# Kernel optimization log

Measured on AMD Instinct MI355X. Metric: run time of the kernel, lower is better.

Reference implementation:

```python
import jax, jax.numpy as jnp
import numpy as np

B, C, H, Wd = 4096, 32, 14, 14
ENC_DIM = 512
ATT_DIM = 128


def setup_inputs() -> dict:
    key = jax.random.key(0)
    ks = jax.random.split(key, 10)
    s = 0.05
    return {
        "img_features": jax.random.normal(ks[0], (B, C, H, Wd), jnp.float32),
        "prev_hidden": jax.random.normal(ks[1], (B, ENC_DIM), jnp.float32),
        "W_w": jax.random.normal(ks[2], (ATT_DIM, C), jnp.float32) * s,
        "W_b": jnp.zeros((ATT_DIM,), jnp.float32),
        "U_w": jax.random.normal(ks[3], (ATT_DIM, ENC_DIM), jnp.float32) * s,
        "U_b": jnp.zeros((ATT_DIM,), jnp.float32),
        "v_w": jax.random.normal(ks[4], (1, ATT_DIM), jnp.float32) * s,
        "v_b": jnp.zeros((1,), jnp.float32),
        "fb_w": jax.random.normal(ks[5], (C, ENC_DIM), jnp.float32) * s,
        "fb_b": jnp.zeros((C,), jnp.float32),
    }


def reference(img_features, prev_hidden, W_w, W_b, U_w, U_b, v_w, v_b, fb_w, fb_b):
    b = img_features.shape[0]
    c = img_features.shape[1]
    # [B, C, H, W] -> [B, P, C] where P = H*W (spatial positions)
    img_parts = img_features.reshape(b, c, -1).transpose(0, 2, 1)
    W_s = jnp.einsum('bpc,ac->bpa', img_parts, W_w) + W_b          # [B, P, 128]
    U_h = prev_hidden @ U_w.T + U_b                                 # [B, 128]
    att = jnp.tanh(W_s + U_h[:, None, :])                           # [B, P, 128]
    score = jnp.einsum('bpa,a->bp', att, v_w[0]) + v_b[0]           # [B, P]
    att_weights = jax.nn.softmax(score, axis=1)                     # softmax over spatial
    context = jnp.einsum('bpc,bp->bc', img_parts, att_weights)      # [B, 32]
    beta = jax.nn.sigmoid(prev_hidden @ fb_w.T + fb_b)              # [B, 32]
    context = context * beta
    return (context, att_weights)
```

## Files before the change

kernel.cpp:

```cpp
#include <hip/hip_runtime.h>
#include <hip/hip_bf16.h>


typedef __attribute__((ext_vector_type(8))) short short8;
typedef __attribute__((ext_vector_type(8))) __bf16 bf16x8;
typedef __attribute__((ext_vector_type(4))) float floatx4;
typedef __attribute__((ext_vector_type(4))) unsigned int uint4v;

static __device__ __forceinline__ float bf2f(unsigned short u) {
    union { unsigned int i; float f; } v; v.i = ((unsigned int)u) << 16; return v.f;
}
static __device__ __forceinline__ unsigned short f2bf(float f) {
    union { float f; unsigned int i; } v; v.f = f;
    unsigned int r = v.i + 0x7FFFu + ((v.i >> 16) & 1u);
    return (unsigned short)(r >> 16);
}
static __device__ __forceinline__ float tanh_rcp(float x) {
    float e = __expf(2.0f * x);
    float r = __builtin_amdgcn_rcpf(1.0f + e);
    return __builtin_fmaf(-2.0f, r, 1.0f);
}
static __device__ __forceinline__ float sigmoid_rcp(float x) {
    return __builtin_amdgcn_rcpf(1.0f + __expf(-x));
}
static __device__ __forceinline__ void split_trunc8(const float* src, bf16x8* hi, bf16x8* lo) {
    uint4v u0 = *(const uint4v*)src;
    uint4v u1 = *(const uint4v*)(src + 4);
    unsigned int fb[8], lb[8];
#pragma unroll
    for (int j = 0; j < 4; j++) { fb[j] = u0[j]; fb[4 + j] = u1[j]; }
#pragma unroll
    for (int k = 0; k < 8; k++) {
        float x = __uint_as_float(fb[k]);
        float h = __uint_as_float(fb[k] & 0xFFFF0000u);
        lb[k] = __float_as_uint(x - h);
    }
    uint4v hp, lp;
#pragma unroll
    for (int j = 0; j < 4; j++) {
        hp[j] = __builtin_amdgcn_perm(fb[2 * j + 1], fb[2 * j], 0x07060302u);
        lp[j] = __builtin_amdgcn_perm(lb[2 * j + 1], lb[2 * j], 0x07060302u);
    }
    *hi = __builtin_bit_cast(bf16x8, hp);
    *lo = __builtin_bit_cast(bf16x8, lp);
}

__global__ __launch_bounds__(256) void k0_split(
    const float* __restrict__ U_w, const float* __restrict__ fb_w,
    const float* __restrict__ W_w,
    unsigned short* __restrict__ Bhi, unsigned short* __restrict__ Blo,
    unsigned short* __restrict__ Whi, unsigned short* __restrict__ Wlo)
{
    int i = blockIdx.x * 256 + threadIdx.x;
    float x;
    if (i < 65536) x = U_w[i];
    else if (i < 81920) x = fb_w[i - 65536];
    else x = W_w[i - 81920];
    unsigned short h = f2bf(x);
    unsigned short l = f2bf(x - bf2f(h));
    if (i < 81920) { Bhi[i] = h; Blo[i] = l; }
    else { Whi[i - 81920] = h; Wlo[i - 81920] = l; }
}

__global__ __launch_bounds__(256) void k1_gemm(
    const float* __restrict__ hidden,
    const unsigned short* __restrict__ Bhi,
    const unsigned short* __restrict__ Blo,
    const float* __restrict__ U_b, const float* __restrict__ W_b,
    const float* __restrict__ fb_b,
    float* __restrict__ uh_out, float* __restrict__ beta_out,
    float* __restrict__ partial, int nsplit, int direct)
{
    __shared__ float s_part[4 * 2560];
    const int tid = threadIdx.x;
    const int wave = tid >> 6, lane = tid & 63, quad = lane >> 4, l16 = lane & 15;
    const int mtile = blockIdx.x / nsplit;
    const int kblock = 512 / nsplit;
    const int ks0 = (blockIdx.x % nsplit) * kblock + wave * (kblock >> 2);
    const int ksteps = kblock >> 7;
    const int arow = mtile * 16 + l16;

    floatx4 acc[10];
#pragma unroll
    for (int i = 0; i < 10; i++) acc[i] = (floatx4)(0.0f);

    for (int ksi = 0; ksi < ksteps; ksi++) {
        const int e0 = ks0 + ksi * 32 + quad * 8;
        bf16x8 ah, al;
        split_trunc8(hidden + (size_t)arow * 512 + e0, &ah, &al);
#pragma unroll
        for (int n = 0; n < 10; n++) {
            const size_t bo = (size_t)(n * 16 + l16) * 512 + e0;
            bf16x8 bh = *(const bf16x8*)(Bhi + bo);
            bf16x8 bl = *(const bf16x8*)(Blo + bo);
            acc[n] = __builtin_amdgcn_mfma_f32_16x16x32_bf16(ah, bl, acc[n], 0, 0, 0);
            acc[n] = __builtin_amdgcn_mfma_f32_16x16x32_bf16(al, bh, acc[n], 0, 0, 0);
            acc[n] = __builtin_amdgcn_mfma_f32_16x16x32_bf16(ah, bh, acc[n], 0, 0, 0);
        }
    }
#pragma unroll
    for (int n = 0; n < 10; n++)
#pragma unroll
        for (int r = 0; r < 4; r++)
            s_part[wave * 2560 + (quad * 4 + r) * 160 + n * 16 + l16] = acc[n][r];
    __syncthreads();

#pragma unroll
    for (int j = 0; j < 10; j++) {
        const int i = tid + j * 256;
        float v = s_part[i] + s_part[2560 + i] + s_part[5120 + i] + s_part[7680 + i];
        if (direct) {
            const int m = mtile * 16 + i / 160, col = i % 160;
            if (col < 128) uh_out[(size_t)m * 128 + col] = v + U_b[col] + W_b[col];
            else beta_out[(size_t)m * 32 + (col - 128)] = sigmoid_rcp(v + fb_b[col - 128]);
        } else {
            partial[(size_t)blockIdx.x * 2560 + i] = v;
        }
    }
}

__global__ __launch_bounds__(256) void k1b_reduce(
    const float* __restrict__ partial,
    const float* __restrict__ U_b, const float* __restrict__ W_b,
    const float* __restrict__ fb_b,
    float* __restrict__ uh_out, float* __restrict__ beta_out, int nsplit)
{
    const int idx = blockIdx.x * 256 + threadIdx.x;
    const int mt = idx / 2560, r = idx % 2560;
    float v = 0.0f;
    for (int s = 0; s < nsplit; s++)
        v += partial[(size_t)(mt * nsplit + s) * 2560 + r];
    const int m = mt * 16 + r / 160, col = r % 160;
    if (col < 128) uh_out[(size_t)m * 128 + col] = v + U_b[col] + W_b[col];
    else beta_out[(size_t)m * 32 + (col - 128)] = sigmoid_rcp(v + fb_b[col - 128]);
}

#define FSTR 36

__global__ __launch_bounds__(256, 4) void k2_attn(
    const float* __restrict__ img,
    const unsigned short* __restrict__ Whi,
    const unsigned short* __restrict__ Wlo,
    const float* __restrict__ v_w,
    const float* __restrict__ uh,
    const float* __restrict__ beta,
    float* __restrict__ out)
{
    __shared__ __align__(16) float s_img[208 * FSTR];
    __shared__ float s_uhv[256];
    __shared__ float s_score[200];
    __shared__ float s_red[8];
    __shared__ float s_ctx[4][32];

    const int tid = threadIdx.x;
    const int b = blockIdx.x;
    const int wave = tid >> 6, lane = tid & 63, quad = lane >> 4, l16 = lane & 15;

    if (tid < 196) {
        const size_t base = (size_t)b * 6272 + tid;
#pragma unroll
        for (int g = 0; g < 8; g++) {
            floatx4 t;
#pragma unroll
            for (int j = 0; j < 4; j++) t[j] = img[base + (size_t)(4 * g + j) * 196];
            *(floatx4*)&s_img[tid * FSTR + 4 * g] = t;
        }
    } else {
        for (int i = tid - 196; i < 12 * FSTR; i += 60) s_img[196 * FSTR + i] = 0.0f;
    }
    if (tid < 128) s_uhv[tid] = uh[(size_t)b * 128 + tid];
    else s_uhv[tid] = v_w[tid - 128];

    bf16x8 bh[8], bl[8];
#pragma unroll
    for (int nt = 0; nt < 8; nt++) {
        const int a = nt * 16 + l16;
        bh[nt] = *(const bf16x8*)(Whi + a * 32 + quad * 8);
        bl[nt] = *(const bf16x8*)(Wlo + a * 32 + quad * 8);
    }
    __syncthreads();

    float ua[8], va[8];
#pragma unroll
    for (int nt = 0; nt < 8; nt++) {
        ua[nt] = s_uhv[nt * 16 + l16];
        va[nt] = s_uhv[128 + nt * 16 + l16];
    }

    for (int mt = wave; mt < 13; mt += 4) {
        const int p_lane = mt * 16 + l16;
        bf16x8 ah, al;
        split_trunc8(&s_img[p_lane * FSTR + quad * 8], &ah, &al);
        float sc[4] = {0.f, 0.f, 0.f, 0.f};
#pragma unroll
        for (int nt = 0; nt < 8; nt++) {
            floatx4 d = (floatx4)(0.0f);
            d = __builtin_amdgcn_mfma_f32_16x16x32_bf16(ah, bl[nt], d, 0, 0, 0);
            d = __builtin_amdgcn_mfma_f32_16x16x32_bf16(al, bh[nt], d, 0, 0, 0);
            d = __builtin_amdgcn_mfma_f32_16x16x32_bf16(ah, bh[nt], d, 0, 0, 0);
#pragma unroll
            for (int r = 0; r < 4; r++)
                sc[r] = __builtin_fmaf(va[nt], tanh_rcp(d[r] + ua[nt]), sc[r]);
        }
#pragma unroll
        for (int r = 0; r < 4; r++) {
            sc[r] += __shfl_xor(sc[r], 1);
            sc[r] += __shfl_xor(sc[r], 2);
            sc[r] += __shfl_xor(sc[r], 4);
            sc[r] += __shfl_xor(sc[r], 8);
        }
        if (l16 == 0) {
#pragma unroll
            for (int r = 0; r < 4; r++) {
                const int p = mt * 16 + quad * 4 + r;
                if (p < 196) s_score[p] = sc[r];
            }
        }
    }
    __syncthreads();

    float x = (tid < 196) ? s_score[tid] : -1e30f;
    float m = x;
#pragma unroll
    for (int off = 32; off > 0; off >>= 1) m = fmaxf(m, __shfl_xor(m, off));
    if (lane == 0) s_red[wave] = m;
    __syncthreads();
    m = fmaxf(fmaxf(s_red[0], s_red[1]), fmaxf(s_red[2], s_red[3]));
    float e = (tid < 196) ? __expf(x - m) : 0.0f;
    float ssum = e;
#pragma unroll
    for (int off = 32; off > 0; off >>= 1) ssum += __shfl_xor(ssum, off);
    if (lane == 0) s_red[4 + wave] = ssum;
    __syncthreads();
    const float tot = s_red[4] + s_red[5] + s_red[6] + s_red[7];
    const float wgt = e * __builtin_amdgcn_rcpf(tot);
    if (tid < 196) {
        s_score[tid] = wgt;
        out[131072 + (size_t)b * 196 + tid] = wgt;
    }
    __syncthreads();

    {
        const int c = lane & 31;
        const int po = wave * 2 + (lane >> 5);
        float acc = 0.0f;
        for (int j = 0; j < 25; j++) {
            const int p = po + j * 8;
            if (p < 196) acc = __builtin_fmaf(s_img[p * FSTR + c], s_score[p], acc);
        }
        acc += __shfl_xor(acc, 32);
        if ((lane >> 5) == 0) s_ctx[wave][c] = acc;
    }
    __syncthreads();
    if (tid < 32) {
        const float v = s_ctx[0][tid] + s_ctx[1][tid] + s_ctx[2][tid] + s_ctx[3][tid];
        out[(size_t)b * 32 + tid] = v * beta[(size_t)b * 32 + tid];
    }
}

extern "C" void kernel_launch(void* const* d_in, const int* in_sizes, int n_in,
                              void* d_out, int out_size, void* d_ws, size_t ws_size,
                              hipStream_t stream) {
    const float* img    = (const float*)d_in[0];
    const float* hidden = (const float*)d_in[1];
    const float* W_w    = (const float*)d_in[2];
    const float* W_b    = (const float*)d_in[3];
    const float* U_w    = (const float*)d_in[4];
    const float* U_b    = (const float*)d_in[5];
    const float* v_w    = (const float*)d_in[6];
    const float* fb_w   = (const float*)d_in[8];
    const float* fb_b   = (const float*)d_in[9];
    float* out = (float*)d_out;

    float* uh_ws   = (float*)d_ws;
    float* beta_ws = uh_ws + 4096 * 128;
    unsigned short* Bhi = (unsigned short*)(beta_ws + 4096 * 32);
    unsigned short* Blo = Bhi + 81920;
    unsigned short* Whi = Blo + 81920;
    unsigned short* Wlo = Whi + 4096;
    float* partial = (float*)(Wlo + 4096);
    const size_t fixed_bytes = ((char*)partial) - ((char*)d_ws);

    int nsplit = 1, direct = 1;
    if (ws_size >= fixed_bytes + (size_t)256 * 4 * 2560 * 4) { nsplit = 4; direct = 0; }
    else if (ws_size >= fixed_bytes + (size_t)256 * 2 * 2560 * 4) { nsplit = 2; direct = 0; }
    else if (ws_size >= fixed_bytes + (size_t)256 * 1 * 2560 * 4) { nsplit = 1; direct = 0; }

    k0_split<<<dim3(336), dim3(256), 0, stream>>>(U_w, fb_w, W_w, Bhi, Blo, Whi, Wlo);
    k1_gemm<<<dim3(256 * nsplit), dim3(256), 0, stream>>>(
        hidden, Bhi, Blo, U_b, W_b, fb_b, uh_ws, beta_ws, partial, nsplit, direct);
    if (!direct)
        k1b_reduce<<<dim3(2560), dim3(256), 0, stream>>>(
            partial, U_b, W_b, fb_b, uh_ws, beta_ws, nsplit);
    k2_attn<<<dim3(4096), dim3(256), 0, stream>>>(img, Whi, Wlo, v_w, uh_ws, beta_ws, out);
}
```

Before: 211.7 us.

## Fold tanh scaling into weights, restructure MFMA loop over m-tiles

```diff
diff --git a/kernel.cpp b/kernel.cpp
--- a/kernel.cpp
+++ b/kernel.cpp
@@ -7,6 +7,14 @@
 typedef __attribute__((ext_vector_type(4))) float floatx4;
 typedef __attribute__((ext_vector_type(4))) unsigned int uint4v;
 
+#define K2E 2.8853900817779268f
+
+#if __has_builtin(__builtin_amdgcn_exp2f)
+#define EXP2F(x) __builtin_amdgcn_exp2f(x)
+#else
+#define EXP2F(x) __expf(0.6931471805599453f * (x))
+#endif
+
 static __device__ __forceinline__ float bf2f(unsigned short u) {
     union { unsigned int i; float f; } v; v.i = ((unsigned int)u) << 16; return v.f;
 }
@@ -15,11 +23,6 @@
     unsigned int r = v.i + 0x7FFFu + ((v.i >> 16) & 1u);
     return (unsigned short)(r >> 16);
 }
-static __device__ __forceinline__ float tanh_rcp(float x) {
-    float e = __expf(2.0f * x);
-    float r = __builtin_amdgcn_rcpf(1.0f + e);
-    return __builtin_fmaf(-2.0f, r, 1.0f);
-}
 static __device__ __forceinline__ float sigmoid_rcp(float x) {
     return __builtin_amdgcn_rcpf(1.0f + __expf(-x));
 }
@@ -43,6 +46,11 @@
     }
     *hi = __builtin_bit_cast(bf16x8, hp);
     *lo = __builtin_bit_cast(bf16x8, lp);
+}
+static __device__ __forceinline__ void pinv(bf16x8& v) {
+    uint4v u = __builtin_bit_cast(uint4v, v);
+    asm volatile("" : "+v"(u));
+    v = __builtin_bit_cast(bf16x8, u);
 }
 
 __global__ __launch_bounds__(256) void k0_split(
@@ -55,7 +63,7 @@
     float x;
     if (i < 65536) x = U_w[i];
     else if (i < 81920) x = fb_w[i - 65536];
-    else x = W_w[i - 81920];
+    else x = W_w[i - 81920] * K2E;
     unsigned short h = f2bf(x);
     unsigned short l = f2bf(x - bf2f(h));
     if (i < 81920) { Bhi[i] = h; Blo[i] = l; }
@@ -64,8 +72,7 @@
 
 __global__ __launch_bounds__(256) void k1_gemm(
     const float* __restrict__ hidden,
-    const unsigned short* __restrict__ Bhi,
-    const unsigned short* __restrict__ Blo,
+    const unsigned short* __restrict__ Bhi, const unsigned short* __restrict__ Blo,
     const float* __restrict__ U_b, const float* __restrict__ W_b,
     const float* __restrict__ fb_b,
     float* __restrict__ uh_out, float* __restrict__ beta_out,
@@ -111,7 +118,7 @@
         float v = s_part[i] + s_part[2560 + i] + s_part[5120 + i] + s_part[7680 + i];
         if (direct) {
             const int m = mtile * 16 + i / 160, col = i % 160;
-            if (col < 128) uh_out[(size_t)m * 128 + col] = v + U_b[col] + W_b[col];
+            if (col < 128) uh_out[(size_t)m * 128 + col] = K2E * (v + U_b[col] + W_b[col]);
             else beta_out[(size_t)m * 32 + (col - 128)] = sigmoid_rcp(v + fb_b[col - 128]);
         } else {
             partial[(size_t)blockIdx.x * 2560 + i] = v;
@@ -131,7 +138,7 @@
     for (int s = 0; s < nsplit; s++)
         v += partial[(size_t)(mt * nsplit + s) * 2560 + r];
     const int m = mt * 16 + r / 160, col = r % 160;
-    if (col < 128) uh_out[(size_t)m * 128 + col] = v + U_b[col] + W_b[col];
+    if (col < 128) uh_out[(size_t)m * 128 + col] = K2E * (v + U_b[col] + W_b[col]);
     else beta_out[(size_t)m * 32 + (col - 128)] = sigmoid_rcp(v + fb_b[col - 128]);
 }
 
@@ -147,8 +154,7 @@
     float* __restrict__ out)
 {
     __shared__ __align__(16) float s_img[208 * FSTR];
-    __shared__ float s_uhv[256];
-    __shared__ float s_score[200];
+    __shared__ float s_score[208];
     __shared__ float s_red[8];
     __shared__ float s_ctx[4][32];
 
@@ -167,53 +173,71 @@
         }
     } else {
         for (int i = tid - 196; i < 12 * FSTR; i += 60) s_img[196 * FSTR + i] = 0.0f;
-    }
-    if (tid < 128) s_uhv[tid] = uh[(size_t)b * 128 + tid];
-    else s_uhv[tid] = v_w[tid - 128];
-
-    bf16x8 bh[8], bl[8];
+        if (tid < 208) s_score[tid] = 0.0f;
+    }
+
+    float uaR[8], va2R[8], sv = 0.0f;
 #pragma unroll
     for (int nt = 0; nt < 8; nt++) {
-        const int a = nt * 16 + l16;
-        bh[nt] = *(const bf16x8*)(Whi + a * 32 + quad * 8);
-        bl[nt] = *(const bf16x8*)(Wlo + a * 32 + quad * 8);
-    }
-    __syncthreads();
-
-    float ua[8], va[8];
+        uaR[nt] = uh[(size_t)b * 128 + nt * 16 + l16];
+        float v = v_w[nt * 16 + l16];
+        sv += v;
+        va2R[nt] = -2.0f * v;
+    }
+    sv += __shfl_xor(sv, 1); sv += __shfl_xor(sv, 2);
+    sv += __shfl_xor(sv, 4); sv += __shfl_xor(sv, 8);
+    __syncthreads();
+
+    const int cnt = (wave == 0) ? 4 : 3;
+    bf16x8 ah[4], al[4];
+#pragma unroll
+    for (int i = 0; i < 4; i++) {
+        if (i < cnt) {
+            const int p_lane = (wave + 4 * i) * 16 + l16;
+            split_trunc8(&s_img[p_lane * FSTR + quad * 8], &ah[i], &al[i]);
+            pinv(ah[i]); pinv(al[i]);
+        }
+    }
+    float sc[4][4];
+#pragma unroll
+    for (int i = 0; i < 4; i++)
+#pragma unroll
+        for (int r = 0; r < 4; r++) sc[i][r] = 0.0f;
+
 #pragma unroll
     for (int nt = 0; nt < 8; nt++) {
-        ua[nt] = s_uhv[nt * 16 + l16];
-        va[nt] = s_uhv[128 + nt * 16 + l16];
-    }
-
-    for (int mt = wave; mt < 13; mt += 4) {
-        const int p_lane = mt * 16 + l16;
-        bf16x8 ah, al;
-        split_trunc8(&s_img[p_lane * FSTR + quad * 8], &ah, &al);
-        float sc[4] = {0.f, 0.f, 0.f, 0.f};
-#pragma unroll
-        for (int nt = 0; nt < 8; nt++) {
-            floatx4 d = (floatx4)(0.0f);
-            d = __builtin_amdgcn_mfma_f32_16x16x32_bf16(ah, bl[nt], d, 0, 0, 0);
-            d = __builtin_amdgcn_mfma_f32_16x16x32_bf16(al, bh[nt], d, 0, 0, 0);
-            d = __builtin_amdgcn_mfma_f32_16x16x32_bf16(ah, bh[nt], d, 0, 0, 0);
-#pragma unroll
-            for (int r = 0; r < 4; r++)
-                sc[r] = __builtin_fmaf(va[nt], tanh_rcp(d[r] + ua[nt]), sc[r]);
-        }
-#pragma unroll
-        for (int r = 0; r < 4; r++) {
-            sc[r] += __shfl_xor(sc[r], 1);
-            sc[r] += __shfl_xor(sc[r], 2);
-            sc[r] += __shfl_xor(sc[r], 4);
-            sc[r] += __shfl_xor(sc[r], 8);
-        }
-        if (l16 == 0) {
+        const int wo = (nt * 16 + l16) * 32 + quad * 8;
+        bf16x8 bh = *(const bf16x8*)(Whi + wo);
+        bf16x8 bl = *(const bf16x8*)(Wlo + wo);
+        const float ua = uaR[nt], w2 = va2R[nt];
+#pragma unroll
+        for (int i = 0; i < 4; i++) {
+            if (i < cnt) {
+                floatx4 d = {ua, ua, ua, ua};
+                d = __builtin_amdgcn_mfma_f32_16x16x32_bf16(ah[i], bl, d, 0, 0, 0);
+                d = __builtin_amdgcn_mfma_f32_16x16x32_bf16(al[i], bh, d, 0, 0, 0);
+                d = __builtin_amdgcn_mfma_f32_16x16x32_bf16(ah[i], bh, d, 0, 0, 0);
+#pragma unroll
+                for (int r = 0; r < 4; r++) {
+                    float e = EXP2F(d[r]);
+                    float rr = __builtin_amdgcn_rcpf(1.0f + e);
+                    sc[i][r] = __builtin_fmaf(w2, rr, sc[i][r]);
+                }
+            }
+        }
+    }
+#pragma unroll
+    for (int i = 0; i < 4; i++) {
+        if (i < cnt) {
 #pragma unroll
             for (int r = 0; r < 4; r++) {
-                const int p = mt * 16 + quad * 4 + r;
-                if (p < 196) s_score[p] = sc[r];
+                float s = sc[i][r];
+                s += __shfl_xor(s, 1); s += __shfl_xor(s, 2);
+                s += __shfl_xor(s, 4); s += __shfl_xor(s, 8);
+                if (l16 == 0) {
+                    const int p = (wave + 4 * i) * 16 + quad * 4 + r;
+                    if (p < 196) s_score[p] = sv + s;
+                }
             }
         }
     }
@@ -244,9 +268,10 @@
         const int c = lane & 31;
         const int po = wave * 2 + (lane >> 5);
         float acc = 0.0f;
+#pragma unroll 5
         for (int j = 0; j < 25; j++) {
             const int p = po + j * 8;
-            if (p < 196) acc = __builtin_fmaf(s_img[p * FSTR + c], s_score[p], acc);
+            acc = __builtin_fmaf(s_img[p * FSTR + c], s_score[p], acc);
         }
         acc += __shfl_xor(acc, 32);
         if ((lane >> 5) == 0) s_ctx[wave][c] = acc;
```

New measurement: 296.8 us. 1.4x slower.
